# Performance work log

Hardware: AMD Instinct MI355X
Metric: run time of the kernel (lower is better)

## Reference

```python
import jax, jax.numpy as jnp
import numpy as np

KS = 11
SIGMA = 1.5
DATA_RANGE = 1.0
CHANNELS = 3
C1 = (0.01 * DATA_RANGE) ** 2
C2 = (0.03 * DATA_RANGE) ** 2
EPS = 1e-08


def _gaussian_kernel():
    k1d = jnp.linspace(-(KS // 2), KS // 2, KS, dtype=jnp.float32)
    k1d = jnp.exp(-(k1d ** 2) / (2.0 * SIGMA ** 2))
    k2d = jnp.outer(k1d, k1d)
    k2d = k2d / k2d.sum()
    # depthwise kernel: (out_ch=C, in_ch/groups=1, KH, KW)
    return jnp.tile(k2d[None, None], (CHANNELS, 1, 1, 1))


def setup_inputs() -> dict:
    key = jax.random.key(0)
    k1, k2 = jax.random.split(key)
    B, C, H, W = 32, CHANNELS, 512, 512
    pred = jax.random.normal(k1, (B, C, H, W), dtype=jnp.float32)
    target = jax.random.normal(k2, (B, C, H, W), dtype=jnp.float32)
    kernel = _gaussian_kernel()
    return {"pred": pred, "target": target, "kernel": kernel}


def _dwconv(x, kernel):
    pad = KS // 2
    return jax.lax.conv_general_dilated(
        x, kernel,
        window_strides=(1, 1),
        padding=((pad, pad), (pad, pad)),
        dimension_numbers=("NCHW", "OIHW", "NCHW"),
        feature_group_count=CHANNELS,
    )


def reference(pred, target, kernel):
    # map from [-1,1] to [0, data_range]
    p = (pred + 1.0) / 2.0 * DATA_RANGE
    t = (target + 1.0) / 2.0 * DATA_RANGE

    mu_x = _dwconv(p, kernel)
    mu_y = _dwconv(t, kernel)
    sigma_x = _dwconv(p * p, kernel) - mu_x * mu_x
    sigma_y = _dwconv(t * t, kernel) - mu_y * mu_y
    sigma_xy = _dwconv(p * t, kernel) - mu_x * mu_y

    num = (2.0 * mu_x * mu_y + C1) * (2.0 * sigma_xy + C2)
    den = (mu_x ** 2 + mu_y ** 2 + C1) * (sigma_x + sigma_y + C2)
    ssim_map = num / (den + EPS)
    return jnp.mean(ssim_map, axis=(1, 2, 3))  # per-image SSIM, shape (B,)
```

## Files before the change

kernel.cpp:

```cpp
#include <hip/hip_runtime.h>

typedef float v2f __attribute__((ext_vector_type(2)));
typedef float v4f __attribute__((ext_vector_type(4)));

#define KS     11
#define HWDIM  512
#define IMG    (HWDIM*HWDIM)
#define TH     32
#define STRIPS 16
#define PLANES 96
#define EG     4
#define EOW    264
#define NPARTIAL (PLANES*STRIPS)

__device__ __forceinline__ float ssim_px(float mu_u, float mu_v, float Su, float Sv)
{
    const float C1v = 1e-4f, C2v = 9e-4f, EPSV = 1e-8f;
    const float uu = mu_u*mu_u, vv = mu_v*mu_v;
    const float mu2d = 0.5f*(uu - vv);
    const float mu2s = 0.5f*(uu + vv);
    const float Sd   = 0.5f*(Su - Sv);
    const float Ss   = 0.5f*(Su + Sv);
    const float A  = mu2d + C1v;
    const float B  = Sd - mu2d + C2v;
    const float Cc = mu2s + C1v;
    const float D  = Ss - mu2s + C2v;
    return A * B * __builtin_amdgcn_rcpf(Cc*D + EPSV);
}

#define LOADUV(Y, A, B) do {                                                  \
    if ((unsigned)(Y) < HWDIM) {                                              \
        const v2f p2 = *(const v2f*)(pR + (size_t)(Y)*HWDIM);                 \
        const v2f t2 = *(const v2f*)(tR + (size_t)(Y)*HWDIM);                 \
        A = (v2f){0.5f*(p2.x + t2.x) + 1.0f, 0.5f*(p2.x - t2.x)};             \
        B = (v2f){0.5f*(p2.y + t2.y) + 1.0f, 0.5f*(p2.y - t2.y)};             \
    } else { A = (v2f)(0.f); B = (v2f)(0.f); }                                \
} while(0)

#define VTAP(W, S) do {                                                       \
    const v2f tA_ = (W) * A##S;                                               \
    mA += tA_;  SA = __builtin_elementwise_fma(tA_, A##S, SA);                \
    const v2f tB_ = (W) * B##S;                                               \
    mB += tB_;  SB = __builtin_elementwise_fma(tB_, B##S, SB);                \
} while(0)

#define HF(ACC, W, T)                                                         \
    ACC = __builtin_elementwise_fma((v4f){(W),(W),(W),(W)}, (T), ACC)

__global__ __launch_bounds__(256) void ssim_stream_kernel(
    const float* __restrict__ pred,
    const float* __restrict__ target,
    const float* __restrict__ kern,
    float* __restrict__ partial)
{
    __shared__ v4f hbufE[2][EOW];
    __shared__ v4f hbufO[2][EOW];
    __shared__ float red[4];

    const int tid   = threadIdx.x;
    const int strip = blockIdx.x;
    const int plane = blockIdx.y;
    const int y0    = strip * TH;

    const float inv_a5 = 1.0f / sqrtf(kern[60]);
    const float w0  = kern[55]*inv_a5,  w1 = kern[56]*inv_a5;
    const float w2  = kern[57]*inv_a5,  w3 = kern[58]*inv_a5;
    const float w4  = kern[59]*inv_a5,  w5 = kern[60]*inv_a5;
    const float w6  = kern[61]*inv_a5,  w7 = kern[62]*inv_a5;
    const float w8  = kern[63]*inv_a5,  w9 = kern[64]*inv_a5;
    const float w10 = kern[65]*inv_a5;

    const float* pR = pred   + (size_t)plane * IMG + 2*tid;
    const float* tR = target + (size_t)plane * IMG + 2*tid;

    if (tid < EG) {
        const v4f z = (v4f)(0.f);
        hbufE[0][tid] = z;                 hbufE[1][tid] = z;
        hbufO[0][tid] = z;                 hbufO[1][tid] = z;
        hbufE[0][EG+256+tid] = z;          hbufE[1][EG+256+tid] = z;
        hbufO[0][EG+256+tid] = z;          hbufO[1][EG+256+tid] = z;
    }

    v2f A0,A1,A2,A3,A4,A5,A6,A7,A8,A9,A10;
    v2f B0,B1,B2,B3,B4,B5,B6,B7,B8,B9,B10;
    v2f nA, nB;

    A0 = (v2f)(0.f); B0 = (v2f)(0.f);
    LOADUV(y0-5, A1, B1);
    LOADUV(y0-4, A2, B2);
    LOADUV(y0-3, A3, B3);
    LOADUV(y0-2, A4, B4);
    LOADUV(y0-1, A5, B5);
    LOADUV(y0+0, A6, B6);
    LOADUV(y0+1, A7, B7);
    LOADUV(y0+2, A8, B8);
    LOADUV(y0+3, A9, B9);
    LOADUV(y0+4, A10, B10);
    LOADUV(y0+5, nA, nB);

    float lsum = 0.f;
    for (int r = 0; r < TH; ++r) {
        A0=A1; B0=B1; A1=A2; B1=B2; A2=A3; B2=B3; A3=A4; B3=B4; A4=A5; B4=B5;
        A5=A6; B5=B6; A6=A7; B6=B7; A7=A8; B7=B8; A8=A9; B8=B9; A9=A10; B9=B10;
        A10=nA; B10=nB;
        LOADUV(y0 + r + 6, nA, nB);

        v2f mA = (v2f)(0.f), SA = (v2f)(0.f);
        v2f mB = (v2f)(0.f), SB = (v2f)(0.f);
        VTAP(w0,0);  VTAP(w1,1);  VTAP(w2,2);  VTAP(w3,3);  VTAP(w4,4);
        VTAP(w5,5);  VTAP(w6,6);  VTAP(w7,7);  VTAP(w8,8);  VTAP(w9,9);
        VTAP(w10,10);

        v4f* bE = &hbufE[r & 1][0];
        v4f* bO = &hbufO[r & 1][0];
        bE[EG + tid] = (v4f){mA.x, mA.y, SA.x, SA.y};
        bO[EG + tid] = (v4f){mB.x, mB.y, SB.x, SB.y};
        __syncthreads();

        v4f accA = (v4f)(0.f), accB = (v4f)(0.f);
        {
            v4f e, o;
            o = bO[EG + tid - 3]; HF(accA, w0,  o);
            e = bE[EG + tid - 2]; HF(accA, w1,  e); HF(accB, w0,  e);
            o = bO[EG + tid - 2]; HF(accA, w2,  o); HF(accB, w1,  o);
            e = bE[EG + tid - 1]; HF(accA, w3,  e); HF(accB, w2,  e);
            o = bO[EG + tid - 1]; HF(accA, w4,  o); HF(accB, w3,  o);
            e = bE[EG + tid    ]; HF(accA, w5,  e); HF(accB, w4,  e);
            o = bO[EG + tid    ]; HF(accA, w6,  o); HF(accB, w5,  o);
            e = bE[EG + tid + 1]; HF(accA, w7,  e); HF(accB, w6,  e);
            o = bO[EG + tid + 1]; HF(accA, w8,  o); HF(accB, w7,  o);
            e = bE[EG + tid + 2]; HF(accA, w9,  e); HF(accB, w8,  e);
            o = bO[EG + tid + 2]; HF(accA, w10, o); HF(accB, w9,  o);
            e = bE[EG + tid + 3];                   HF(accB, w10, e);
        }
        lsum += ssim_px(accA.x, accA.y, accA.z, accA.w);
        lsum += ssim_px(accB.x, accB.y, accB.z, accB.w);
    }

    #pragma unroll
    for (int off = 32; off > 0; off >>= 1)
        lsum += __shfl_down(lsum, off, 64);
    if ((tid & 63) == 0) red[tid >> 6] = lsum;
    __syncthreads();
    if (tid == 0)
        partial[plane * STRIPS + strip] = red[0] + red[1] + red[2] + red[3];
}

__global__ __launch_bounds__(64) void ssim_reduce_kernel(
    const float* __restrict__ partial,
    float* __restrict__ out)
{
    const int b    = blockIdx.x;
    const int lane = threadIdx.x;
    float s = (lane < 48) ? partial[b * 48 + lane] : 0.f;
    #pragma unroll
    for (int off = 32; off > 0; off >>= 1)
        s += __shfl_down(s, off, 64);
    if (lane == 0) out[b] = s * (1.0f / (3.0f * 512.0f * 512.0f));
}

extern "C" void kernel_launch(void* const* d_in, const int* in_sizes, int n_in,
                              void* d_out, int out_size, void* d_ws, size_t ws_size,
                              hipStream_t stream) {
    (void)in_sizes; (void)n_in; (void)out_size; (void)ws_size;
    const float* pred   = (const float*)d_in[0];
    const float* target = (const float*)d_in[1];
    const float* kern   = (const float*)d_in[2];
    float* out     = (float*)d_out;
    float* partial = (float*)d_ws;

    dim3 grid(STRIPS, PLANES);
    ssim_stream_kernel<<<grid, 256, 0, stream>>>(pred, target, kern, partial);
    ssim_reduce_kernel<<<32, 64, 0, stream>>>(partial, out);
}
```

Measured before the change: 98.77 us.

## Process four columns per thread with 128-thread blocks and shorter row strips

Each thread now loads float4 from pred and target and handles four adjacent columns, so blocks shrink to 128 threads. The horizontal pass reads 14 LDS vectors for four outputs instead of 12 for two, which cuts LDS traffic per pixel. Strip height halves to 16 rows and the strip count doubles, so more blocks run but more halo rows are reloaded. Register pressure roughly doubles from the larger sliding window, which may lower occupancy.

```diff
diff --git a/kernel.cpp b/kernel.cpp
--- a/kernel.cpp
+++ b/kernel.cpp
@@ -6,11 +6,11 @@
 #define KS     11
 #define HWDIM  512
 #define IMG    (HWDIM*HWDIM)
-#define TH     32
-#define STRIPS 16
+#define TH     16
+#define STRIPS 32
 #define PLANES 96
-#define EG     4
-#define EOW    264
+#define EG2    2
+#define QW     132
 #define NPARTIAL (PLANES*STRIPS)
 
 __device__ __forceinline__ float ssim_px(float mu_u, float mu_v, float Su, float Sv)
@@ -28,34 +28,36 @@
     return A * B * __builtin_amdgcn_rcpf(Cc*D + EPSV);
 }
 
-#define LOADUV(Y, A, B) do {                                                  \
+#define LOADUV(Y, A, B, C, D) do {                                            \
     if ((unsigned)(Y) < HWDIM) {                                              \
-        const v2f p2 = *(const v2f*)(pR + (size_t)(Y)*HWDIM);                 \
-        const v2f t2 = *(const v2f*)(tR + (size_t)(Y)*HWDIM);                 \
-        A = (v2f){0.5f*(p2.x + t2.x) + 1.0f, 0.5f*(p2.x - t2.x)};             \
-        B = (v2f){0.5f*(p2.y + t2.y) + 1.0f, 0.5f*(p2.y - t2.y)};             \
-    } else { A = (v2f)(0.f); B = (v2f)(0.f); }                                \
+        const v4f p4 = *(const v4f*)(pR + (size_t)(Y)*HWDIM);                 \
+        const v4f t4 = *(const v4f*)(tR + (size_t)(Y)*HWDIM);                 \
+        A = (v2f){0.5f*(p4.x + t4.x) + 1.0f, 0.5f*(p4.x - t4.x)};             \
+        B = (v2f){0.5f*(p4.y + t4.y) + 1.0f, 0.5f*(p4.y - t4.y)};             \
+        C = (v2f){0.5f*(p4.z + t4.z) + 1.0f, 0.5f*(p4.z - t4.z)};             \
+        D = (v2f){0.5f*(p4.w + t4.w) + 1.0f, 0.5f*(p4.w - t4.w)};             \
+    } else { A=(v2f)(0.f); B=(v2f)(0.f); C=(v2f)(0.f); D=(v2f)(0.f); }        \
 } while(0)
 
 #define VTAP(W, S) do {                                                       \
-    const v2f tA_ = (W) * A##S;                                               \
-    mA += tA_;  SA = __builtin_elementwise_fma(tA_, A##S, SA);                \
-    const v2f tB_ = (W) * B##S;                                               \
-    mB += tB_;  SB = __builtin_elementwise_fma(tB_, B##S, SB);                \
+    v2f t_;                                                                   \
+    t_ = (W)*A##S; mA += t_; SA = __builtin_elementwise_fma(t_, A##S, SA);    \
+    t_ = (W)*B##S; mB += t_; SB = __builtin_elementwise_fma(t_, B##S, SB);    \
+    t_ = (W)*C##S; mC += t_; SC = __builtin_elementwise_fma(t_, C##S, SC);    \
+    t_ = (W)*D##S; mD += t_; SD = __builtin_elementwise_fma(t_, D##S, SD);    \
 } while(0)
 
 #define HF(ACC, W, T)                                                         \
     ACC = __builtin_elementwise_fma((v4f){(W),(W),(W),(W)}, (T), ACC)
 
-__global__ __launch_bounds__(256) void ssim_stream_kernel(
+__global__ __launch_bounds__(128) void ssim_stream_kernel(
     const float* __restrict__ pred,
     const float* __restrict__ target,
     const float* __restrict__ kern,
     float* __restrict__ partial)
 {
-    __shared__ v4f hbufE[2][EOW];
-    __shared__ v4f hbufO[2][EOW];
-    __shared__ float red[4];
+    __shared__ v4f Pq[2][4][QW];
+    __shared__ float red[2];
 
     const int tid   = threadIdx.x;
     const int strip = blockIdx.x;
@@ -70,71 +72,89 @@
     const float w8  = kern[63]*inv_a5,  w9 = kern[64]*inv_a5;
     const float w10 = kern[65]*inv_a5;
 
-    const float* pR = pred   + (size_t)plane * IMG + 2*tid;
-    const float* tR = target + (size_t)plane * IMG + 2*tid;
+    const float* pR = pred   + (size_t)plane * IMG + 4*tid;
+    const float* tR = target + (size_t)plane * IMG + 4*tid;
 
-    if (tid < EG) {
+    if (tid < EG2) {
         const v4f z = (v4f)(0.f);
-        hbufE[0][tid] = z;                 hbufE[1][tid] = z;
-        hbufO[0][tid] = z;                 hbufO[1][tid] = z;
-        hbufE[0][EG+256+tid] = z;          hbufE[1][EG+256+tid] = z;
-        hbufO[0][EG+256+tid] = z;          hbufO[1][EG+256+tid] = z;
+        #pragma unroll
+        for (int par = 0; par < 2; ++par)
+            #pragma unroll
+            for (int k = 0; k < 4; ++k) {
+                Pq[par][k][tid] = z;
+                Pq[par][k][EG2 + 128 + tid] = z;
+            }
     }
 
     v2f A0,A1,A2,A3,A4,A5,A6,A7,A8,A9,A10;
     v2f B0,B1,B2,B3,B4,B5,B6,B7,B8,B9,B10;
-    v2f nA, nB;
+    v2f C0,C1,C2,C3,C4,C5,C6,C7,C8,C9,C10;
+    v2f D0,D1,D2,D3,D4,D5,D6,D7,D8,D9,D10;
+    v2f nA, nB, nC, nD;
 
-    A0 = (v2f)(0.f); B0 = (v2f)(0.f);
-    LOADUV(y0-5, A1, B1);
-    LOADUV(y0-4, A2, B2);
-    LOADUV(y0-3, A3, B3);
-    LOADUV(y0-2, A4, B4);
-    LOADUV(y0-1, A5, B5);
-    LOADUV(y0+0, A6, B6);
-    LOADUV(y0+1, A7, B7);
-    LOADUV(y0+2, A8, B8);
-    LOADUV(y0+3, A9, B9);
-    LOADUV(y0+4, A10, B10);
-    LOADUV(y0+5, nA, nB);
+    A0=(v2f)(0.f); B0=(v2f)(0.f); C0=(v2f)(0.f); D0=(v2f)(0.f);
+    LOADUV(y0-5, A1, B1, C1, D1);
+    LOADUV(y0-4, A2, B2, C2, D2);
+    LOADUV(y0-3, A3, B3, C3, D3);
+    LOADUV(y0-2, A4, B4, C4, D4);
+    LOADUV(y0-1, A5, B5, C5, D5);
+    LOADUV(y0+0, A6, B6, C6, D6);
+    LOADUV(y0+1, A7, B7, C7, D7);
+    LOADUV(y0+2, A8, B8, C8, D8);
+    LOADUV(y0+3, A9, B9, C9, D9);
+    LOADUV(y0+4, A10, B10, C10, D10);
+    LOADUV(y0+5, nA, nB, nC, nD);
 
     float lsum = 0.f;
     for (int r = 0; r < TH; ++r) {
-        A0=A1; B0=B1; A1=A2; B1=B2; A2=A3; B2=B3; A3=A4; B3=B4; A4=A5; B4=B5;
-        A5=A6; B5=B6; A6=A7; B6=B7; A7=A8; B7=B8; A8=A9; B8=B9; A9=A10; B9=B10;
-        A10=nA; B10=nB;
-        LOADUV(y0 + r + 6, nA, nB);
+        A0=A1; B0=B1; C0=C1; D0=D1;
+        A1=A2; B1=B2; C1=C2; D1=D2;
+        A2=A3; B2=B3; C2=C3; D2=D3;
+        A3=A4; B3=B4; C3=C4; D3=D4;
+        A4=A5; B4=B5; C4=C5; D4=D5;
+        A5=A6; B5=B6; C5=C6; D5=D6;
+        A6=A7; B6=B7; C6=C7; D6=D7;
+        A7=A8; B7=B8; C7=C8; D7=D8;
+        A8=A9; B8=B9; C8=C9; D8=D9;
+        A9=A10; B9=B10; C9=C10; D9=D10;
+        A10=nA; B10=nB; C10=nC; D10=nD;
+        LOADUV(y0 + r + 6, nA, nB, nC, nD);
 
-        v2f mA = (v2f)(0.f), SA = (v2f)(0.f);
-        v2f mB = (v2f)(0.f), SB = (v2f)(0.f);
+        v2f mA=(v2f)(0.f), SA=(v2f)(0.f), mB=(v2f)(0.f), SB=(v2f)(0.f);
+        v2f mC=(v2f)(0.f), SC=(v2f)(0.f), mD=(v2f)(0.f), SD=(v2f)(0.f);
         VTAP(w0,0);  VTAP(w1,1);  VTAP(w2,2);  VTAP(w3,3);  VTAP(w4,4);
         VTAP(w5,5);  VTAP(w6,6);  VTAP(w7,7);  VTAP(w8,8);  VTAP(w9,9);
         VTAP(w10,10);
 
-        v4f* bE = &hbufE[r & 1][0];
-        v4f* bO = &hbufO[r & 1][0];
-        bE[EG + tid] = (v4f){mA.x, mA.y, SA.x, SA.y};
-        bO[EG + tid] = (v4f){mB.x, mB.y, SB.x, SB.y};
+        v4f (*P)[QW] = Pq[r & 1];
+        P[0][EG2 + tid] = (v4f){mA.x, mA.y, SA.x, SA.y};
+        P[1][EG2 + tid] = (v4f){mB.x, mB.y, SB.x, SB.y};
+        P[2][EG2 + tid] = (v4f){mC.x, mC.y, SC.x, SC.y};
+        P[3][EG2 + tid] = (v4f){mD.x, mD.y, SD.x, SD.y};
         __syncthreads();
 
-        v4f accA = (v4f)(0.f), accB = (v4f)(0.f);
+        v4f ac0=(v4f)(0.f), ac1=(v4f)(0.f), ac2=(v4f)(0.f), ac3=(v4f)(0.f);
         {
-            v4f e, o;
-            o = bO[EG + tid - 3]; HF(accA, w0,  o);
-            e = bE[EG + tid - 2]; HF(accA, w1,  e); HF(accB, w0,  e);
-            o = bO[EG + tid - 2]; HF(accA, w2,  o); HF(accB, w1,  o);
-            e = bE[EG + tid - 1]; HF(accA, w3,  e); HF(accB, w2,  e);
-            o = bO[EG + tid - 1]; HF(accA, w4,  o); HF(accB, w3,  o);
-            e = bE[EG + tid    ]; HF(accA, w5,  e); HF(accB, w4,  e);
-            o = bO[EG + tid    ]; HF(accA, w6,  o); HF(accB, w5,  o);
-            e = bE[EG + tid + 1]; HF(accA, w7,  e); HF(accB, w6,  e);
-            o = bO[EG + tid + 1]; HF(accA, w8,  o); HF(accB, w7,  o);
-            e = bE[EG + tid + 2]; HF(accA, w9,  e); HF(accB, w8,  e);
-            o = bO[EG + tid + 2]; HF(accA, w10, o); HF(accB, w9,  o);
-            e = bE[EG + tid + 3];                   HF(accB, w10, e);
+            v4f q;
+            q = P[3][EG2+tid-2]; HF(ac0,w0,q);
+            q = P[0][EG2+tid-1]; HF(ac0,w1,q); HF(ac1,w0,q);
+            q = P[1][EG2+tid-1]; HF(ac0,w2,q); HF(ac1,w1,q); HF(ac2,w0,q);
+            q = P[2][EG2+tid-1]; HF(ac0,w3,q); HF(ac1,w2,q); HF(ac2,w1,q); HF(ac3,w0,q);
+            q = P[3][EG2+tid-1]; HF(ac0,w4,q); HF(ac1,w3,q); HF(ac2,w2,q); HF(ac3,w1,q);
+            q = P[0][EG2+tid  ]; HF(ac0,w5,q); HF(ac1,w4,q); HF(ac2,w3,q); HF(ac3,w2,q);
+            q = P[1][EG2+tid  ]; HF(ac0,w6,q); HF(ac1,w5,q); HF(ac2,w4,q); HF(ac3,w3,q);
+            q = P[2][EG2+tid  ]; HF(ac0,w7,q); HF(ac1,w6,q); HF(ac2,w5,q); HF(ac3,w4,q);
+            q = P[3][EG2+tid  ]; HF(ac0,w8,q); HF(ac1,w7,q); HF(ac2,w6,q); HF(ac3,w5,q);
+            q = P[0][EG2+tid+1]; HF(ac0,w9,q); HF(ac1,w8,q); HF(ac2,w7,q); HF(ac3,w6,q);
+            q = P[1][EG2+tid+1]; HF(ac0,w10,q);HF(ac1,w9,q); HF(ac2,w8,q); HF(ac3,w7,q);
+            q = P[2][EG2+tid+1];               HF(ac1,w10,q);HF(ac2,w9,q); HF(ac3,w8,q);
+            q = P[3][EG2+tid+1];                             HF(ac2,w10,q);HF(ac3,w9,q);
+            q = P[0][EG2+tid+2];                                           HF(ac3,w10,q);
         }
-        lsum += ssim_px(accA.x, accA.y, accA.z, accA.w);
-        lsum += ssim_px(accB.x, accB.y, accB.z, accB.w);
+        lsum += ssim_px(ac0.x, ac0.y, ac0.z, ac0.w);
+        lsum += ssim_px(ac1.x, ac1.y, ac1.z, ac1.w);
+        lsum += ssim_px(ac2.x, ac2.y, ac2.z, ac2.w);
+        lsum += ssim_px(ac3.x, ac3.y, ac3.z, ac3.w);
     }
 
     #pragma unroll
@@ -143,7 +163,7 @@
     if ((tid & 63) == 0) red[tid >> 6] = lsum;
     __syncthreads();
     if (tid == 0)
-        partial[plane * STRIPS + strip] = red[0] + red[1] + red[2] + red[3];
+        partial[plane * STRIPS + strip] = red[0] + red[1];
 }
 
 __global__ __launch_bounds__(64) void ssim_reduce_kernel(
@@ -152,7 +172,8 @@
 {
     const int b    = blockIdx.x;
     const int lane = threadIdx.x;
-    float s = (lane < 48) ? partial[b * 48 + lane] : 0.f;
+    float s = partial[b * 96 + lane];
+    if (lane < 32) s += partial[b * 96 + 64 + lane];
     #pragma unroll
     for (int off = 32; off > 0; off >>= 1)
         s += __shfl_down(s, off, 64);
@@ -170,6 +191,6 @@
     float* partial = (float*)d_ws;
 
     dim3 grid(STRIPS, PLANES);
-    ssim_stream_kernel<<<grid, 256, 0, stream>>>(pred, target, kern, partial);
+    ssim_stream_kernel<<<grid, 128, 0, stream>>>(pred, target, kern, partial);
     ssim_reduce_kernel<<<32, 64, 0, stream>>>(partial, out);
 }
```

New measurement: 109.4 us. 1.11x slower.
